# Performance work log

Measured on AMD Instinct MI355X. Metric: run time of the kernel, lower is better.

The kernel has to match this reference:

```python
import jax, jax.numpy as jnp
import numpy as np

K = 7          # kernel_size
D = 1          # dilation
P = (D * (K - 1) + 1) // 2  # reflect padding = 3
N = 2
C_IN = 256
REL = 16
OUT = 256
SHARE = 8
H = 56
W = 56


def _unfold(x, k=K, d=D, p=P):
    # x: [n, c, h, w] -> [n, c, k*k, h*w], reflection-padded local windows
    n, c, h, w = x.shape
    xp = jnp.pad(x, ((0, 0), (0, 0), (p, p), (p, p)), mode='reflect')
    cols = [xp[:, :, i * d:i * d + h, j * d:j * d + w]
            for i in range(k) for j in range(k)]
    return jnp.stack(cols, axis=2).reshape(n, c, k * k, h * w)


def _conv1x1(x, w, b=None):
    # 1x1 conv == channel contraction; x: [n, c, *spatial]
    y = jnp.einsum('oc,nc...->no...', w, x)
    if b is not None:
        y = y + b.reshape((1, -1) + (1,) * (y.ndim - 2))
    return y


def _bn(x, g, b, eps=1e-5):
    # training-mode batchnorm over (N, *spatial) per channel; x: [n, c, a, b]
    m = x.mean(axis=(0, 2, 3), keepdims=True)
    v = x.var(axis=(0, 2, 3), keepdims=True)
    xh = (x - m) * jax.lax.rsqrt(v + eps)
    return xh * g.reshape(1, -1, 1, 1) + b.reshape(1, -1, 1, 1)


def _position(h, w):
    lw = jnp.broadcast_to(jnp.linspace(-1.0, 1.0, w)[None, :], (h, w))
    lh = jnp.broadcast_to(jnp.linspace(-1.0, 1.0, h)[:, None], (h, w))
    return jnp.stack([lw, lh], 0)[None]  # [1, 2, h, w]


def setup_inputs() -> dict:
    key = jax.random.key(0)
    ks = jax.random.split(key, 16)
    def rn(k, shape, s=0.05):
        return jax.random.normal(k, shape, jnp.float32) * s
    return dict(
        x=jax.random.normal(ks[0], (N, C_IN, H, W), jnp.float32),
        w1=rn(ks[1], (REL, C_IN)), b1=rn(ks[2], (REL,)),
        w2=rn(ks[3], (REL, C_IN)), b2=rn(ks[4], (REL,)),
        w3=rn(ks[5], (OUT, C_IN)), b3=rn(ks[6], (OUT,)),
        wp=rn(ks[7], (2, 2)), bp=rn(ks[8], (2,)),
        g1=jnp.ones(REL + 2, jnp.float32), be1=jnp.zeros(REL + 2, jnp.float32),
        cw1=rn(ks[9], (REL, REL + 2)),
        g2=jnp.ones(REL, jnp.float32), be2=jnp.zeros(REL, jnp.float32),
        cw2=rn(ks[10], (OUT // SHARE, REL)), cb2=rn(ks[11], (OUT // SHARE,)),
    )


def reference(x, w1, b1, w2, b2, w3, b3, wp, bp,
              g1, be1, cw1, g2, be2, cw2, cb2):
    n, _, h, w = x.shape
    hw = h * w
    x1 = _conv1x1(x, w1, b1)   # [n, rel, h, w]
    x2 = _conv1x1(x, w2, b2)   # [n, rel, h, w]
    x3 = _conv1x1(x, w3, b3)   # [n, out, h, w]
    pos = _conv1x1(_position(h, w), wp, bp)  # [1, 2, h, w]
    # Subtraction2: center query minus unfolded keys -> [n, rel, k^2, hw]
    sub2 = x1.reshape(n, REL, 1, hw) - _unfold(x2)
    # Subtraction on position: center minus neighbors -> [1, 2, k^2, hw]
    subp = pos.reshape(1, 2, 1, hw) - _unfold(pos)
    subp = jnp.broadcast_to(subp, (n, 2, K * K, hw))
    t = jnp.concatenate([sub2, subp], axis=1)           # [n, rel+2, k^2, hw]
    t = jax.nn.relu(_bn(t, g1, be1))
    t = _conv1x1(t, cw1)                                # [n, rel, k^2, hw]
    t = jax.nn.relu(_bn(t, g2, be2))
    wlog = _conv1x1(t, cw2, cb2)                        # [n, out//share, k^2, hw]
    ww = jax.nn.softmax(wlog, axis=-2)                  # softmax over k^2
    # Aggregation: gather values over windows and weight per share-group
    u3 = _unfold(x3).reshape(n, OUT // SHARE, SHARE, K * K, hw)
    out = jnp.einsum('ngskq,ngkq->ngsq', u3, ww).reshape(n, OUT, h, w)
    return out
```

## Files before the change

### kernel.cpp

```cpp
#include <hip/hip_runtime.h>
#include <hip/hip_bf16.h>
#include <cstdint>
#include <math.h>

#define HWS 3136
#define WID 56
#define NKQ 307328.0f
#define X3SCALE 2048.0f
#define X3INV   (1.0f / 2048.0f)
#define WQ      65535.0f

#define S_CW1 0
#define S_CW2 288
#define S_CB2 800
#define S_WP  832
#define S_G1  836
#define S_BE1 854
#define S_G2  872
#define S_BE2 888
#define S_TOT 904

__device__ __forceinline__ int refl(int i) {
  if (i < 0) i = -i;
  if (i >= WID) i = 2 * WID - 2 - i;
  return i;
}

__global__ __launch_bounds__(256) void k_prep(
    const float* __restrict__ cw1, const float* __restrict__ cw2,
    const float* __restrict__ cb2, const float* __restrict__ wp,
    const float* __restrict__ g1, const float* __restrict__ be1,
    const float* __restrict__ g2, const float* __restrict__ be2,
    float* __restrict__ small)
{
  int e = blockIdx.x * 256 + threadIdx.x;
  if (e >= S_TOT) return;
  float v;
  if (e < S_CW2)      v = cw1[e];
  else if (e < S_CB2) v = cw2[e - S_CW2];
  else if (e < S_WP)  v = cb2[e - S_CB2];
  else if (e < S_G1)  v = wp [e - S_WP];
  else if (e < S_BE1) v = g1 [e - S_G1];
  else if (e < S_G2)  v = be1[e - S_BE1];
  else if (e < S_BE2) v = g2 [e - S_G2];
  else                v = be2[e - S_BE2];
  small[e] = v;
}

__global__ __launch_bounds__(256) void k_proj(
    const float* __restrict__ x,
    const float* __restrict__ w1, const float* __restrict__ b1,
    const float* __restrict__ w2, const float* __restrict__ b2,
    const float* __restrict__ w3, const float* __restrict__ b3,
    float* __restrict__ x1t, float* __restrict__ x2t, short* __restrict__ x3i)
{
  __shared__ float xs[256][8];
  const int tid = threadIdx.x;
  const int n = blockIdx.x / 392;
  const int q0 = (blockIdx.x % 392) * 8;

  for (int e = tid; e < 512; e += 256) {
    int c = e >> 1, h = (e & 1) * 4;
    float4 f = *(const float4*)(x + (size_t)(n * 256 + c) * HWS + q0 + h);
    xs[c][h + 0] = f.x; xs[c][h + 1] = f.y;
    xs[c][h + 2] = f.z; xs[c][h + 3] = f.w;
  }
  __syncthreads();

  for (int idx = tid; idx < 288; idx += 256) {
    const float* wrow; float bias;
    if (idx < 16)      { wrow = w1 + idx * 256;        bias = b1[idx]; }
    else if (idx < 32) { wrow = w2 + (idx - 16) * 256; bias = b2[idx - 16]; }
    else               { wrow = w3 + (idx - 32) * 256; bias = b3[idx - 32]; }
    float acc[8];
    #pragma unroll
    for (int p = 0; p < 8; p++) acc[p] = bias;
    for (int c0 = 0; c0 < 256; c0 += 4) {
      float4 w4 = *(const float4*)(wrow + c0);
      float wv[4] = {w4.x, w4.y, w4.z, w4.w};
      #pragma unroll
      for (int cc = 0; cc < 4; cc++) {
        const float4* xp = (const float4*)(&xs[c0 + cc][0]);
        float4 a = xp[0], b = xp[1];
        acc[0] = fmaf(wv[cc], a.x, acc[0]); acc[1] = fmaf(wv[cc], a.y, acc[1]);
        acc[2] = fmaf(wv[cc], a.z, acc[2]); acc[3] = fmaf(wv[cc], a.w, acc[3]);
        acc[4] = fmaf(wv[cc], b.x, acc[4]); acc[5] = fmaf(wv[cc], b.y, acc[5]);
        acc[6] = fmaf(wv[cc], b.z, acc[6]); acc[7] = fmaf(wv[cc], b.w, acc[7]);
      }
    }
    if (idx < 16) {
      #pragma unroll
      for (int p = 0; p < 8; p++) x1t[(size_t)(n * HWS + q0 + p) * 16 + idx] = acc[p];
    } else if (idx < 32) {
      #pragma unroll
      for (int p = 0; p < 8; p++) x2t[(size_t)(n * HWS + q0 + p) * 16 + (idx - 16)] = acc[p];
    } else {
      #pragma unroll
      for (int p = 0; p < 8; p++) {
        float cl = fminf(fmaxf(acc[p], -15.9f), 15.9f);
        x3i[(size_t)(n * HWS + q0 + p) * 256 + (idx - 32)] = (short)__float2int_rn(cl * X3SCALE);
      }
    }
  }
}

__global__ __launch_bounds__(256) void k_stats1(
    const float* __restrict__ x1t, const float* __restrict__ x2t,
    const float* __restrict__ small, float* __restrict__ gsum1)
{
  __shared__ float red[4][36];
  const int tid = threadIdx.x;
  const int bid = blockIdx.x;
  const int n = bid / 98;
  const int r = bid % 98;
  const int k = r >> 1, half = r & 1;
  const int ki = k / 7 - 3, kj = k % 7 - 3;
  const float wp00 = small[S_WP+0], wp01 = small[S_WP+1];
  const float wp10 = small[S_WP+2], wp11 = small[S_WP+3];
  float s[18], ss[18];
  #pragma unroll
  for (int i = 0; i < 18; i++) { s[i] = 0.f; ss[i] = 0.f; }

  for (int qq = tid; qq < 1568; qq += 256) {
    int q = half * 1568 + qq;
    int y = q / WID, xx = q - y * WID;
    int ny = refl(y + ki), nx = refl(xx + kj);
    int nb = ny * WID + nx;
    const float4* a = (const float4*)(x1t + (size_t)(n * HWS + q) * 16);
    const float4* b = (const float4*)(x2t + (size_t)(n * HWS + nb) * 16);
    #pragma unroll
    for (int r4 = 0; r4 < 4; r4++) {
      float4 av = a[r4], bv = b[r4];
      float v;
      v = av.x - bv.x; s[r4*4+0] += v; ss[r4*4+0] += v * v;
      v = av.y - bv.y; s[r4*4+1] += v; ss[r4*4+1] += v * v;
      v = av.z - bv.z; s[r4*4+2] += v; ss[r4*4+2] += v * v;
      v = av.w - bv.w; s[r4*4+3] += v; ss[r4*4+3] += v * v;
    }
    float dlw = (float)(xx - nx) * (2.f / 55.f);
    float dlh = (float)(y - ny) * (2.f / 55.f);
    float v16 = wp00 * dlw + wp01 * dlh;
    float v17 = wp10 * dlw + wp11 * dlh;
    s[16] += v16; ss[16] += v16 * v16;
    s[17] += v17; ss[17] += v17 * v17;
  }

  #pragma unroll
  for (int i = 0; i < 18; i++) {
    #pragma unroll
    for (int off = 32; off > 0; off >>= 1) {
      s[i]  += __shfl_down(s[i], off);
      ss[i] += __shfl_down(ss[i], off);
    }
  }
  const int wvv = tid >> 6, lane = tid & 63;
  if (lane == 0) {
    #pragma unroll
    for (int i = 0; i < 18; i++) { red[wvv][i] = s[i]; red[wvv][18 + i] = ss[i]; }
  }
  __syncthreads();
  if (tid < 36) {
    float t = red[0][tid] + red[1][tid] + red[2][tid] + red[3][tid];
    atomicAdd(&gsum1[tid], t);
  }
}

__global__ __launch_bounds__(256) void k_stats2(
    const float* __restrict__ x1t, const float* __restrict__ x2t,
    const float* __restrict__ small,
    const float* __restrict__ gsum1, float* __restrict__ gsum2)
{
  __shared__ float red[4][32];
  const int tid = threadIdx.x;
  const float inv = 1.f / NKQ;
  float sc1r[18], sh1r[18];
  #pragma unroll
  for (int c = 0; c < 18; c++) {
    float m = gsum1[c] * inv;
    float var = gsum1[18 + c] * inv - m * m;
    float sc = small[S_G1 + c] * rsqrtf(var + 1e-5f);
    sc1r[c] = sc; sh1r[c] = small[S_BE1 + c] - m * sc;
  }

  const int bid = blockIdx.x;
  const int n = bid / 98;
  const int r = bid % 98;
  const int k = r >> 1, half = r & 1;
  const int ki = k / 7 - 3, kj = k % 7 - 3;
  const float wp00 = small[S_WP+0], wp01 = small[S_WP+1];
  const float wp10 = small[S_WP+2], wp11 = small[S_WP+3];
  const float* cw1f = small + S_CW1;
  float s[16], ss[16];
  #pragma unroll
  for (int i = 0; i < 16; i++) { s[i] = 0.f; ss[i] = 0.f; }

  for (int qq = tid; qq < 1568; qq += 256) {
    int q = half * 1568 + qq;
    int y = q / WID, xx = q - y * WID;
    int ny = refl(y + ki), nx = refl(xx + kj);
    int nb = ny * WID + nx;
    float t1v[18];
    const float4* a4 = (const float4*)(x1t + (size_t)(n * HWS + q) * 16);
    const float4* b4 = (const float4*)(x2t + (size_t)(n * HWS + nb) * 16);
    #pragma unroll
    for (int r4 = 0; r4 < 4; r4++) {
      float4 av = a4[r4], bv = b4[r4];
      t1v[r4*4+0] = av.x - bv.x; t1v[r4*4+1] = av.y - bv.y;
      t1v[r4*4+2] = av.z - bv.z; t1v[r4*4+3] = av.w - bv.w;
    }
    float dlw = (float)(xx - nx) * (2.f / 55.f);
    float dlh = (float)(y - ny) * (2.f / 55.f);
    t1v[16] = wp00 * dlw + wp01 * dlh;
    t1v[17] = wp10 * dlw + wp11 * dlh;
    #pragma unroll
    for (int c = 0; c < 18; c++) t1v[c] = fmaxf(fmaf(t1v[c], sc1r[c], sh1r[c]), 0.f);
    #pragma unroll
    for (int r2 = 0; r2 < 16; r2++) {
      float acc = 0.f;
      #pragma unroll
      for (int c = 0; c < 18; c++) acc = fmaf(cw1f[r2 * 18 + c], t1v[c], acc);
      s[r2] += acc; ss[r2] += acc * acc;
    }
  }

  #pragma unroll
  for (int i = 0; i < 16; i++) {
    #pragma unroll
    for (int off = 32; off > 0; off >>= 1) {
      s[i]  += __shfl_down(s[i], off);
      ss[i] += __shfl_down(ss[i], off);
    }
  }
  const int wvv = tid >> 6, lane = tid & 63;
  if (lane == 0) {
    #pragma unroll
    for (int i = 0; i < 16; i++) { red[wvv][i] = s[i]; red[wvv][16 + i] = ss[i]; }
  }
  __syncthreads();
  if (tid < 32) {
    float t = red[0][tid] + red[1][tid] + red[2][tid] + red[3][tid];
    atomicAdd(&gsum2[tid], t);
  }
}

__global__ __launch_bounds__(256) void k_final(
    const float* __restrict__ x1t, const float* __restrict__ x2t,
    const short* __restrict__ x3i, const float* __restrict__ small,
    const float* __restrict__ gsum1, const float* __restrict__ gsum2,
    float* __restrict__ outf)
{
  __shared__ unsigned short wws[4][49][34];
  __shared__ int nbs[4][49];
  __shared__ float sc1s[18], sh1s[18], sc2s[16], sh2s[16];

  const int tid = threadIdx.x;
  const int lane = tid & 63;
  const int wv = tid >> 6;
  const float inv = 1.f / NKQ;

  if (tid < 18) {
    float m = gsum1[tid] * inv;
    float var = gsum1[18 + tid] * inv - m * m;
    float sc = small[S_G1 + tid] * rsqrtf(var + 1e-5f);
    sc1s[tid] = sc; sh1s[tid] = small[S_BE1 + tid] - m * sc;
  } else if (tid >= 32 && tid < 48) {
    int c = tid - 32;
    float m = gsum2[c] * inv;
    float var = gsum2[16 + c] * inv - m * m;
    float sc = small[S_G2 + c] * rsqrtf(var + 1e-5f);
    sc2s[c] = sc; sh2s[c] = small[S_BE2 + c] - m * sc;
  }
  __syncthreads();

  const int P = blockIdx.x * 4 + wv;
  const int n = P / HWS, q = P % HWS;
  const int y = q / WID, xx = q - y * WID;

  const bool valid = lane < 49;
  const int kk = valid ? lane : 48;
  const int ki = kk / 7 - 3, kj = kk % 7 - 3;
  const int ny = refl(y + ki), nx = refl(xx + kj);
  const int nb = ny * WID + nx;
  if (valid) nbs[wv][lane] = nb;

  float t1v[18];
  {
    const float* a = x1t + (size_t)(n * HWS + q) * 16;
    const float* b = x2t + (size_t)(n * HWS + nb) * 16;
    #pragma unroll
    for (int c = 0; c < 16; c++) t1v[c] = a[c] - b[c];
    float dlw = (float)(xx - nx) * (2.f / 55.f);
    float dlh = (float)(y - ny) * (2.f / 55.f);
    t1v[16] = small[S_WP+0] * dlw + small[S_WP+1] * dlh;
    t1v[17] = small[S_WP+2] * dlw + small[S_WP+3] * dlh;
  }
  #pragma unroll
  for (int c = 0; c < 18; c++)
    t1v[c] = fmaxf(fmaf(t1v[c], sc1s[c], sh1s[c]), 0.f);

  float t2v[16];
  #pragma unroll
  for (int r = 0; r < 16; r++) {
    float acc = 0.f;
    #pragma unroll
    for (int c = 0; c < 18; c++) acc = fmaf(small[S_CW1 + r * 18 + c], t1v[c], acc);
    t2v[r] = fmaxf(fmaf(acc, sc2s[r], sh2s[r]), 0.f);
  }

  #pragma unroll
  for (int g = 0; g < 32; g++) {
    float acc = small[S_CB2 + g];
    #pragma unroll
    for (int r = 0; r < 16; r++) acc = fmaf(small[S_CW2 + g * 16 + r], t2v[r], acc);
    float e = valid ? __expf(acc) : 0.f;
    float s = e;
    #pragma unroll
    for (int off = 32; off >= 1; off >>= 1) s += __shfl_xor(s, off);
    if (valid)
      wws[wv][lane][g] = (unsigned short)__float2uint_rn(e / s * WQ);
  }
  __syncthreads();

  const short* x3p = x3i + (size_t)n * HWS * 256;
  const int* nbp = nbs[wv];
  const unsigned short (*wq)[34] = wws[wv];
  const int g0 = lane >> 3;
  float acc4[4] = {0.f, 0.f, 0.f, 0.f};
  #pragma unroll 7
  for (int k = 0; k < 49; k++) {
    const short* row = x3p + (size_t)nbp[k] * 256;
    #pragma unroll
    for (int ch = 0; ch < 4; ch++) {
      float w = (float)wq[k][ch * 8 + g0];
      acc4[ch] = fmaf(w, (float)row[ch * 64 + lane], acc4[ch]);
    }
  }
  const float osc = X3INV / WQ;
  #pragma unroll
  for (int ch = 0; ch < 4; ch++) {
    int o = ch * 64 + lane;
    outf[(size_t)(n * 256 + o) * HWS + q] = acc4[ch] * osc;
  }
}

extern "C" void kernel_launch(void* const* d_in, const int* in_sizes, int n_in,
                              void* d_out, int out_size, void* d_ws, size_t ws_size,
                              hipStream_t stream) {
  (void)in_sizes; (void)n_in; (void)out_size; (void)ws_size;
  char* ws = (char*)d_ws;
  float* gsum1 = (float*)(ws + 0);
  float* gsum2 = (float*)(ws + 160);
  float* small = (float*)(ws + 512);
  float* x1t   = (float*)(ws + 4608);
  float* x2t   = (float*)(ws + 406016);
  short* x3i   = (short*)(ws + 807424);
  float* outf  = (float*)d_out;

  const float* x   = (const float*)d_in[0];
  const float* w1  = (const float*)d_in[1];
  const float* b1  = (const float*)d_in[2];
  const float* w2  = (const float*)d_in[3];
  const float* b2  = (const float*)d_in[4];
  const float* w3  = (const float*)d_in[5];
  const float* b3  = (const float*)d_in[6];
  const float* wp  = (const float*)d_in[7];
  const float* g1  = (const float*)d_in[9];
  const float* be1 = (const float*)d_in[10];
  const float* cw1 = (const float*)d_in[11];
  const float* g2  = (const float*)d_in[12];
  const float* be2 = (const float*)d_in[13];
  const float* cw2 = (const float*)d_in[14];
  const float* cb2 = (const float*)d_in[15];

  hipMemsetAsync(d_ws, 0, 512, stream);
  k_prep<<<4, 256, 0, stream>>>(cw1, cw2, cb2, wp, g1, be1, g2, be2, small);
  k_proj<<<784, 256, 0, stream>>>(x, w1, b1, w2, b2, w3, b3, x1t, x2t, x3i);
  k_stats1<<<196, 256, 0, stream>>>(x1t, x2t, small, gsum1);
  k_stats2<<<196, 256, 0, stream>>>(x1t, x2t, small, gsum1, gsum2);
  k_final<<<1568, 256, 0, stream>>>(x1t, x2t, x3i, small, gsum1, gsum2, outf);
}
```

Before: 200.4 us.

## Register-tile projection GEMM with staged weights; split stats kernels into quarters

The projection kernel now has each block cover 32 pixels with 128 threads. Each thread computes a 9-output-row by 8-pixel register tile, and weight chunks are staged through shared memory, so weights are reused across pixels instead of being re-read from global memory by every thread. Both stats kernels move from halves to quarters of the spatial range, doubling their grid to 392 blocks for better occupancy. The final kernel now reads x1/x2 with float4 vector loads. In exchange, the projection launch is much smaller (196 blocks of 128 threads) and uses 72 accumulator registers per thread, which may lower occupancy.

```diff
diff --git a/kernel.cpp b/kernel.cpp
--- a/kernel.cpp
+++ b/kernel.cpp
@@ -1,7 +1,6 @@
 #include <hip/hip_runtime.h>
 #include <hip/hip_bf16.h>
 #include <cstdint>
-#include <math.h>
 
 #define HWS 3136
 #define WID 56
@@ -47,58 +46,87 @@
   small[e] = v;
 }
 
-__global__ __launch_bounds__(256) void k_proj(
+__global__ __launch_bounds__(128) void k_proj(
     const float* __restrict__ x,
     const float* __restrict__ w1, const float* __restrict__ b1,
     const float* __restrict__ w2, const float* __restrict__ b2,
     const float* __restrict__ w3, const float* __restrict__ b3,
     float* __restrict__ x1t, float* __restrict__ x2t, short* __restrict__ x3i)
 {
-  __shared__ float xs[256][8];
+  __shared__ float xs[256][32];
+  __shared__ float wc[16][32][12];
   const int tid = threadIdx.x;
-  const int n = blockIdx.x / 392;
-  const int q0 = (blockIdx.x % 392) * 8;
-
-  for (int e = tid; e < 512; e += 256) {
-    int c = e >> 1, h = (e & 1) * 4;
-    float4 f = *(const float4*)(x + (size_t)(n * 256 + c) * HWS + q0 + h);
-    xs[c][h + 0] = f.x; xs[c][h + 1] = f.y;
-    xs[c][h + 2] = f.z; xs[c][h + 3] = f.w;
-  }
-  __syncthreads();
-
-  for (int idx = tid; idx < 288; idx += 256) {
-    const float* wrow; float bias;
-    if (idx < 16)      { wrow = w1 + idx * 256;        bias = b1[idx]; }
-    else if (idx < 32) { wrow = w2 + (idx - 16) * 256; bias = b2[idx - 16]; }
-    else               { wrow = w3 + (idx - 32) * 256; bias = b3[idx - 32]; }
-    float acc[8];
-    #pragma unroll
-    for (int p = 0; p < 8; p++) acc[p] = bias;
-    for (int c0 = 0; c0 < 256; c0 += 4) {
-      float4 w4 = *(const float4*)(wrow + c0);
-      float wv[4] = {w4.x, w4.y, w4.z, w4.w};
-      #pragma unroll
-      for (int cc = 0; cc < 4; cc++) {
-        const float4* xp = (const float4*)(&xs[c0 + cc][0]);
-        float4 a = xp[0], b = xp[1];
-        acc[0] = fmaf(wv[cc], a.x, acc[0]); acc[1] = fmaf(wv[cc], a.y, acc[1]);
-        acc[2] = fmaf(wv[cc], a.z, acc[2]); acc[3] = fmaf(wv[cc], a.w, acc[3]);
-        acc[4] = fmaf(wv[cc], b.x, acc[4]); acc[5] = fmaf(wv[cc], b.y, acc[5]);
-        acc[6] = fmaf(wv[cc], b.z, acc[6]); acc[7] = fmaf(wv[cc], b.w, acc[7]);
-      }
-    }
-    if (idx < 16) {
-      #pragma unroll
-      for (int p = 0; p < 8; p++) x1t[(size_t)(n * HWS + q0 + p) * 16 + idx] = acc[p];
-    } else if (idx < 32) {
-      #pragma unroll
-      for (int p = 0; p < 8; p++) x2t[(size_t)(n * HWS + q0 + p) * 16 + (idx - 16)] = acc[p];
+  const int n  = blockIdx.x / 98;
+  const int q0 = (blockIdx.x % 98) * 32;
+  const int t  = tid & 31;
+  const int p0 = (tid >> 5) * 8;
+
+  for (int e = tid; e < 2048; e += 128) {
+    int c = e >> 3, p4 = (e & 7) * 4;
+    float4 f = *(const float4*)(x + (size_t)(n * 256 + c) * HWS + q0 + p4);
+    xs[c][p4 + 0] = f.x; xs[c][p4 + 1] = f.y;
+    xs[c][p4 + 2] = f.z; xs[c][p4 + 3] = f.w;
+  }
+
+  float acc[9][8];
+  #pragma unroll
+  for (int i = 0; i < 9; i++) {
+    int r = 9 * t + i;
+    float bias = (r < 16) ? b1[r] : (r < 32) ? b2[r - 16] : b3[r - 32];
+    #pragma unroll
+    for (int p = 0; p < 8; p++) acc[i][p] = bias;
+  }
+
+  for (int ch = 0; ch < 16; ch++) {
+    __syncthreads();
+    const int c0 = ch * 16;
+    for (int e = tid; e < 1152; e += 128) {
+      int row = e >> 2, jq = (e & 3) * 4;
+      const float* src;
+      if (row < 16)      src = w1 + row * 256;
+      else if (row < 32) src = w2 + (row - 16) * 256;
+      else               src = w3 + (row - 32) * 256;
+      float4 f = *(const float4*)(src + c0 + jq);
+      int tt = row / 9, ii = row - tt * 9;
+      wc[jq + 0][tt][ii] = f.x;
+      wc[jq + 1][tt][ii] = f.y;
+      wc[jq + 2][tt][ii] = f.z;
+      wc[jq + 3][tt][ii] = f.w;
+    }
+    __syncthreads();
+    #pragma unroll
+    for (int j = 0; j < 16; j++) {
+      float w9[9], x8[8];
+      #pragma unroll
+      for (int i = 0; i < 9; i++) w9[i] = wc[j][t][i];
+      const float* xr = &xs[c0 + j][p0];
+      #pragma unroll
+      for (int p = 0; p < 8; p++) x8[p] = xr[p];
+      #pragma unroll
+      for (int i = 0; i < 9; i++)
+        #pragma unroll
+        for (int p = 0; p < 8; p++)
+          acc[i][p] = fmaf(w9[i], x8[p], acc[i][p]);
+    }
+  }
+
+  #pragma unroll
+  for (int i = 0; i < 9; i++) {
+    int r = 9 * t + i;
+    if (r < 16) {
+      #pragma unroll
+      for (int p = 0; p < 8; p++)
+        x1t[(size_t)(n * HWS + q0 + p0 + p) * 16 + r] = acc[i][p];
+    } else if (r < 32) {
+      #pragma unroll
+      for (int p = 0; p < 8; p++)
+        x2t[(size_t)(n * HWS + q0 + p0 + p) * 16 + (r - 16)] = acc[i][p];
     } else {
       #pragma unroll
       for (int p = 0; p < 8; p++) {
-        float cl = fminf(fmaxf(acc[p], -15.9f), 15.9f);
-        x3i[(size_t)(n * HWS + q0 + p) * 256 + (idx - 32)] = (short)__float2int_rn(cl * X3SCALE);
+        float cl = fminf(fmaxf(acc[i][p], -15.9f), 15.9f);
+        x3i[(size_t)(n * HWS + q0 + p0 + p) * 256 + (r - 32)] =
+            (short)__float2int_rn(cl * X3SCALE);
       }
     }
   }
@@ -111,9 +139,9 @@
   __shared__ float red[4][36];
   const int tid = threadIdx.x;
   const int bid = blockIdx.x;
-  const int n = bid / 98;
-  const int r = bid % 98;
-  const int k = r >> 1, half = r & 1;
+  const int n = bid / 196;
+  const int r = bid % 196;
+  const int k = r >> 2, quar = r & 3;
   const int ki = k / 7 - 3, kj = k % 7 - 3;
   const float wp00 = small[S_WP+0], wp01 = small[S_WP+1];
   const float wp10 = small[S_WP+2], wp11 = small[S_WP+3];
@@ -121,8 +149,8 @@
   #pragma unroll
   for (int i = 0; i < 18; i++) { s[i] = 0.f; ss[i] = 0.f; }
 
-  for (int qq = tid; qq < 1568; qq += 256) {
-    int q = half * 1568 + qq;
+  for (int qq = tid; qq < 784; qq += 256) {
+    int q = quar * 784 + qq;
     int y = q / WID, xx = q - y * WID;
     int ny = refl(y + ki), nx = refl(xx + kj);
     int nb = ny * WID + nx;
@@ -183,9 +211,9 @@
   }
 
   const int bid = blockIdx.x;
-  const int n = bid / 98;
-  const int r = bid % 98;
-  const int k = r >> 1, half = r & 1;
+  const int n = bid / 196;
+  const int r = bid % 196;
+  const int k = r >> 2, quar = r & 3;
   const int ki = k / 7 - 3, kj = k % 7 - 3;
   const float wp00 = small[S_WP+0], wp01 = small[S_WP+1];
   const float wp10 = small[S_WP+2], wp11 = small[S_WP+3];
@@ -194,8 +222,8 @@
   #pragma unroll
   for (int i = 0; i < 16; i++) { s[i] = 0.f; ss[i] = 0.f; }
 
-  for (int qq = tid; qq < 1568; qq += 256) {
-    int q = half * 1568 + qq;
+  for (int qq = tid; qq < 784; qq += 256) {
+    int q = quar * 784 + qq;
     int y = q / WID, xx = q - y * WID;
     int ny = refl(y + ki), nx = refl(xx + kj);
     int nb = ny * WID + nx;
@@ -285,10 +313,14 @@
 
   float t1v[18];
   {
-    const float* a = x1t + (size_t)(n * HWS + q) * 16;
-    const float* b = x2t + (size_t)(n * HWS + nb) * 16;
-    #pragma unroll
-    for (int c = 0; c < 16; c++) t1v[c] = a[c] - b[c];
+    const float4* a4 = (const float4*)(x1t + (size_t)(n * HWS + q) * 16);
+    const float4* b4 = (const float4*)(x2t + (size_t)(n * HWS + nb) * 16);
+    #pragma unroll
+    for (int r4 = 0; r4 < 4; r4++) {
+      float4 av = a4[r4], bv = b4[r4];
+      t1v[r4*4+0] = av.x - bv.x; t1v[r4*4+1] = av.y - bv.y;
+      t1v[r4*4+2] = av.z - bv.z; t1v[r4*4+3] = av.w - bv.w;
+    }
     float dlw = (float)(xx - nx) * (2.f / 55.f);
     float dlh = (float)(y - ny) * (2.f / 55.f);
     t1v[16] = small[S_WP+0] * dlw + small[S_WP+1] * dlh;
@@ -374,8 +406,8 @@
 
   hipMemsetAsync(d_ws, 0, 512, stream);
   k_prep<<<4, 256, 0, stream>>>(cw1, cw2, cb2, wp, g1, be1, g2, be2, small);
-  k_proj<<<784, 256, 0, stream>>>(x, w1, b1, w2, b2, w3, b3, x1t, x2t, x3i);
-  k_stats1<<<196, 256, 0, stream>>>(x1t, x2t, small, gsum1);
-  k_stats2<<<196, 256, 0, stream>>>(x1t, x2t, small, gsum1, gsum2);
+  k_proj<<<196, 128, 0, stream>>>(x, w1, b1, w2, b2, w3, b3, x1t, x2t, x3i);
+  k_stats1<<<392, 256, 0, stream>>>(x1t, x2t, small, gsum1);
+  k_stats2<<<392, 256, 0, stream>>>(x1t, x2t, small, gsum1, gsum2);
   k_final<<<1568, 256, 0, stream>>>(x1t, x2t, x3i, small, gsum1, gsum2, outf);
 }
```

Result: slower. 238.4 us (+19.0%).
